# Performance work log

Measured on AMD Instinct MI355X. Metric: run time of the kernel, lower is better.

The kernel has to match this reference:

```python
import jax, jax.numpy as jnp
import numpy as np

FP32_MIN_NORMAL = 2.0 ** -126
BLOCK = 128
STD_DEV = 2.0
# inlier format int4: ebits=0, mbits=4+2, emax=0, max_norm=(2^5-1)/2^4
EBITS_IN, MBITS_IN, EMAX_IN, MAXNORM_IN = 0, 6, 0, (2 ** 5 - 1) / 2 ** 4
# outlier format fp8_e4m3: ebits=4, mbits=3+2, emax=2^3, max_norm=2^8*1.75
EBITS_OUT, MBITS_OUT, EMAX_OUT, MAXNORM_OUT = 4, 5, 8, 448.0
SCALE_EMAX = 2 ** (8 - 1) - 1  # inlier/outlier scale_bits = 8
SCALE_LO = -20.0  # original: lower clamp is -20 because -scale_emax < -20


def setup_inputs():
    key = jax.random.key(0)
    x = jax.random.normal(key, (4096, 8192), dtype=jnp.float32)
    return {"x": x}


def _quantize_elemwise(A, mbits, ebits, max_norm):
    # faithful to microxcaling _quantize_elemwise_core with allow_denorm=True,
    # saturate_normals=True, round='nearest' (finite inputs assumed)
    if ebits != 0:
        pexp = jnp.floor(jnp.log2(jnp.abs(A) + (A == 0).astype(A.dtype)))
        pexp = jnp.maximum(pexp, float(-(2 ** (ebits - 1)) + 2))
        scale = jnp.exp2(float(mbits - 2) - pexp)
    else:
        scale = float(2 ** (mbits - 2))
    out = A * scale
    out = jnp.sign(out) * jnp.floor(jnp.abs(out) + 0.5)  # round-to-nearest
    out = out / scale
    return jnp.clip(out, -max_norm, max_norm)


def _shared_exp(A):
    # max-abs over the block axis, then floor(log2(.)), zero-safe
    m = jnp.max(jnp.abs(A), axis=-1, keepdims=True)
    return jnp.floor(jnp.log2(m + FP32_MIN_NORMAL * (m == 0).astype(m.dtype)))


def _clamp_scale(se):
    se = jnp.where(se > SCALE_EMAX, jnp.nan, se)  # never triggers for fp32-range data
    return jnp.where(se < -SCALE_EMAX, SCALE_LO, se)


def _quantize_mx_outlier(x):
    R, C = x.shape  # C divisible by BLOCK -> no padding branch
    A = x.reshape(R, C // BLOCK, BLOCK)
    # outlier detection: mean/std of |A| per block (population std), bounds vs A
    absA = jnp.abs(A)
    mean = jnp.mean(absA, axis=-1, keepdims=True)
    std = jnp.sqrt(jnp.mean((absA - mean) ** 2, axis=-1, keepdims=True))
    outlier = ((A < mean - STD_DEV * std) | (A > mean + STD_DEV * std)).astype(A.dtype)
    inlier_val = A * (1.0 - outlier)
    outlier_val = A * outlier
    # inlier shared exponent + quantize
    se_in = _clamp_scale(_shared_exp(inlier_val) - EMAX_IN)
    s_in = jnp.exp2(se_in)
    inlier_val = _quantize_elemwise(inlier_val / s_in, MBITS_IN, EBITS_IN, MAXNORM_IN) * s_in
    # outlier path (note: scaled UP by inlier scale, as in original)
    outlier_val = outlier_val * s_in
    se_out = _clamp_scale(_shared_exp(outlier_val) - EMAX_OUT)
    s_out = jnp.exp2(se_out)
    outlier_val = _quantize_elemwise(outlier_val / s_out, MBITS_OUT, EBITS_OUT, MAXNORM_OUT) * s_out / s_in
    return (inlier_val + outlier_val).reshape(R, C)


def reference(x):
    return _quantize_mx_outlier(x)
```

## Files before the change

kernel.cpp:

```cpp
#include <hip/hip_runtime.h>

typedef float f32x4 __attribute__((ext_vector_type(4)));

__device__ __forceinline__ int flog2_exact(float x) {
    unsigned b = __float_as_uint(x);
    int e = (int)((b >> 23) & 0xFFu);
    if (e == 0) {
        unsigned m = b & 0x7FFFFFu;
        return 31 - __clz(m) - 149;
    }
    return e - 127;
}

__device__ __forceinline__ float round_ref(float v) {
    return copysignf(floorf(fabsf(v) + 0.5f), v);
}

__global__ __launch_bounds__(256) void mxq_kernel(const f32x4* __restrict__ x,
                                                  f32x4* __restrict__ y,
                                                  int ntask) {
    const int lane = threadIdx.x & 63;
    const int l    = lane & 15;
    const int q    = lane >> 4;
    const int wid  = blockIdx.x * (blockDim.x >> 6) + (threadIdx.x >> 6);
    const int nw   = gridDim.x * (blockDim.x >> 6);

    for (int t = wid; t < ntask; t += nw) {
        const size_t base = (size_t)t * 128 + q * 32 + l;
        const f32x4 v0 = x[base];
        const f32x4 v1 = x[base + 16];
        float a[8] = {v0.x, v0.y, v0.z, v0.w, v1.x, v1.y, v1.z, v1.w};

        double s = 0.0, s2 = 0.0;
        #pragma unroll
        for (int i = 0; i < 8; ++i) {
            double d = (double)fabsf(a[i]);
            s += d;
            s2 = fma(d, d, s2);
        }
        #pragma unroll
        for (int off = 1; off < 16; off <<= 1) {
            s  += __shfl_xor(s, off);
            s2 += __shfl_xor(s2, off);
        }
        const double mean = s * (1.0 / 128.0);
        double var = fma(mean, -mean, s2 * (1.0 / 128.0));
        var = var < 0.0 ? 0.0 : var;
        const double v4 = 4.0 * var;

        bool o[8];
        float mi = 0.0f, mov = 0.0f;
        #pragma unroll
        for (int i = 0; i < 8; ++i) {
            double dd = (double)a[i] - mean;
            o[i] = fma(dd, dd, -v4) > 0.0;
            float ab = fabsf(a[i]);
            mi  = fmaxf(mi,  o[i] ? 0.0f : ab);
            mov = fmaxf(mov, o[i] ? ab : 0.0f);
        }
        #pragma unroll
        for (int off = 1; off < 16; off <<= 1) {
            mi  = fmaxf(mi,  __shfl_xor(mi, off));
            mov = fmaxf(mov, __shfl_xor(mov, off));
        }

        int se_in = (mi == 0.0f) ? -126 : flog2_exact(mi);
        if (se_in < -127) se_in = -20;
        int se_out = ((mov == 0.0f) ? -126 : (flog2_exact(mov) + se_in)) - 8;
        if (se_out < -127) se_out = -20;
        const int d   = se_in - se_out;
        const int g_in = se_in - 4;
        const float L_in  = ldexpf(31.0f, g_in);
        const float L_out = ldexpf(448.0f, -d);
        const int d3 = d + 3;

        f32x4 r0, r1;
        #pragma unroll
        for (int i = 0; i < 8; ++i) {
            int e_a = (int)((__float_as_uint(a[i]) >> 23) & 0xFFu) - 127;
            int pe  = e_a + d;
            pe = pe < -6 ? -6 : pe;
            int g = o[i] ? (pe - d3) : g_in;
            float r    = round_ref(ldexpf(a[i], -g));
            float outv = ldexpf(r, g);
            float L    = o[i] ? L_out : L_in;
            outv = fminf(fmaxf(outv, -L), L);
            if (i < 4) r0[i] = outv; else r1[i - 4] = outv;
        }

        __builtin_nontemporal_store(r0, &y[base]);
        __builtin_nontemporal_store(r1, &y[base + 16]);
    }
}

extern "C" void kernel_launch(void* const* d_in, const int* in_sizes, int n_in,
                              void* d_out, int out_size, void* d_ws, size_t ws_size,
                              hipStream_t stream) {
    const f32x4* x = (const f32x4*)d_in[0];
    f32x4* y = (f32x4*)d_out;
    int n = in_sizes[0];
    int ntask = n / 512;
    int threads = 256;
    int waves_per_wg = threads / 64;
    int grid = 2048;
    int max_grid = (ntask + waves_per_wg - 1) / waves_per_wg;
    if (grid > max_grid) grid = max_grid;
    mxq_kernel<<<grid, threads, 0, stream>>>(x, y, ntask);
}
```

Measured before the change: 46.07 us.

## Process two tasks per wave iteration with register double-buffered prefetch

Each wave now handles a super-task of two 128-element rows per iteration (8 f32x4 loads in flight) and prefetches the next super-task's data into registers before computing the current one. The aim is to hide global memory latency in this bandwidth-bound kernel and raise memory-level parallelism per wave. The cost is higher register pressure, which may lower occupancy, and half as many tasks to spread across waves.

```diff
diff --git a/kernel.cpp b/kernel.cpp
--- a/kernel.cpp
+++ b/kernel.cpp
@@ -16,80 +16,101 @@
     return copysignf(floorf(fabsf(v) + 0.5f), v);
 }
 
+__device__ __forceinline__ void process_task(const f32x4 v0, const f32x4 v1,
+                                             f32x4& r0, f32x4& r1) {
+    float a[8] = {v0.x, v0.y, v0.z, v0.w, v1.x, v1.y, v1.z, v1.w};
+
+    double s = 0.0, s2 = 0.0;
+    #pragma unroll
+    for (int i = 0; i < 8; ++i) {
+        double d = (double)fabsf(a[i]);
+        s += d;
+        s2 = fma(d, d, s2);
+    }
+    #pragma unroll
+    for (int off = 1; off < 16; off <<= 1) {
+        s  += __shfl_xor(s, off);
+        s2 += __shfl_xor(s2, off);
+    }
+    const double mean = s * (1.0 / 128.0);
+    double var = fma(mean, -mean, s2 * (1.0 / 128.0));
+    var = var < 0.0 ? 0.0 : var;
+    const double v4 = 4.0 * var;
+
+    bool o[8];
+    float mi = 0.0f, mov = 0.0f;
+    #pragma unroll
+    for (int i = 0; i < 8; ++i) {
+        double dd = (double)a[i] - mean;
+        o[i] = fma(dd, dd, -v4) > 0.0;
+        float ab = fabsf(a[i]);
+        mi  = fmaxf(mi,  o[i] ? 0.0f : ab);
+        mov = fmaxf(mov, o[i] ? ab : 0.0f);
+    }
+    #pragma unroll
+    for (int off = 1; off < 16; off <<= 1) {
+        mi  = fmaxf(mi,  __shfl_xor(mi, off));
+        mov = fmaxf(mov, __shfl_xor(mov, off));
+    }
+
+    int se_in = (mi == 0.0f) ? -126 : flog2_exact(mi);
+    if (se_in < -127) se_in = -20;
+    int se_out = ((mov == 0.0f) ? -126 : (flog2_exact(mov) + se_in)) - 8;
+    if (se_out < -127) se_out = -20;
+    const int d   = se_in - se_out;
+    const int g_in = se_in - 4;
+    const float L_in  = ldexpf(31.0f, g_in);
+    const float L_out = ldexpf(448.0f, -d);
+    const int d3 = d + 3;
+
+    #pragma unroll
+    for (int i = 0; i < 8; ++i) {
+        int e_a = (int)((__float_as_uint(a[i]) >> 23) & 0xFFu) - 127;
+        int pe  = e_a + d;
+        pe = pe < -6 ? -6 : pe;
+        int g = o[i] ? (pe - d3) : g_in;
+        float r    = round_ref(ldexpf(a[i], -g));
+        float outv = ldexpf(r, g);
+        float L    = o[i] ? L_out : L_in;
+        outv = fminf(fmaxf(outv, -L), L);
+        if (i < 4) r0[i] = outv; else r1[i - 4] = outv;
+    }
+}
+
 __global__ __launch_bounds__(256) void mxq_kernel(const f32x4* __restrict__ x,
                                                   f32x4* __restrict__ y,
-                                                  int ntask) {
+                                                  int nsuper) {
     const int lane = threadIdx.x & 63;
-    const int l    = lane & 15;
-    const int q    = lane >> 4;
+    const int off0 = (lane >> 4) * 32 + (lane & 15);
     const int wid  = blockIdx.x * (blockDim.x >> 6) + (threadIdx.x >> 6);
     const int nw   = gridDim.x * (blockDim.x >> 6);
 
-    for (int t = wid; t < ntask; t += nw) {
-        const size_t base = (size_t)t * 128 + q * 32 + l;
-        const f32x4 v0 = x[base];
-        const f32x4 v1 = x[base + 16];
-        float a[8] = {v0.x, v0.y, v0.z, v0.w, v1.x, v1.y, v1.z, v1.w};
-
-        double s = 0.0, s2 = 0.0;
-        #pragma unroll
-        for (int i = 0; i < 8; ++i) {
-            double d = (double)fabsf(a[i]);
-            s += d;
-            s2 = fma(d, d, s2);
-        }
-        #pragma unroll
-        for (int off = 1; off < 16; off <<= 1) {
-            s  += __shfl_xor(s, off);
-            s2 += __shfl_xor(s2, off);
-        }
-        const double mean = s * (1.0 / 128.0);
-        double var = fma(mean, -mean, s2 * (1.0 / 128.0));
-        var = var < 0.0 ? 0.0 : var;
-        const double v4 = 4.0 * var;
-
-        bool o[8];
-        float mi = 0.0f, mov = 0.0f;
-        #pragma unroll
-        for (int i = 0; i < 8; ++i) {
-            double dd = (double)a[i] - mean;
-            o[i] = fma(dd, dd, -v4) > 0.0;
-            float ab = fabsf(a[i]);
-            mi  = fmaxf(mi,  o[i] ? 0.0f : ab);
-            mov = fmaxf(mov, o[i] ? ab : 0.0f);
-        }
-        #pragma unroll
-        for (int off = 1; off < 16; off <<= 1) {
-            mi  = fmaxf(mi,  __shfl_xor(mi, off));
-            mov = fmaxf(mov, __shfl_xor(mov, off));
+    int t = wid;
+    f32x4 d0, d1, d2, d3;
+    if (t < nsuper) {
+        const size_t b = (size_t)t * 256 + off0;
+        d0 = x[b]; d1 = x[b + 16]; d2 = x[b + 128]; d3 = x[b + 144];
+    }
+    while (t < nsuper) {
+        const int tn = t + nw;
+        f32x4 e0 = d0, e1 = d1, e2 = d2, e3 = d3;
+        if (tn < nsuper) {
+            const size_t bn = (size_t)tn * 256 + off0;
+            e0 = x[bn]; e1 = x[bn + 16]; e2 = x[bn + 128]; e3 = x[bn + 144];
         }
 
-        int se_in = (mi == 0.0f) ? -126 : flog2_exact(mi);
-        if (se_in < -127) se_in = -20;
-        int se_out = ((mov == 0.0f) ? -126 : (flog2_exact(mov) + se_in)) - 8;
-        if (se_out < -127) se_out = -20;
-        const int d   = se_in - se_out;
-        const int g_in = se_in - 4;
-        const float L_in  = ldexpf(31.0f, g_in);
-        const float L_out = ldexpf(448.0f, -d);
-        const int d3 = d + 3;
+        f32x4 r0, r1, r2, r3;
+        process_task(d0, d1, r0, r1);
+        process_task(d2, d3, r2, r3);
 
-        f32x4 r0, r1;
-        #pragma unroll
-        for (int i = 0; i < 8; ++i) {
-            int e_a = (int)((__float_as_uint(a[i]) >> 23) & 0xFFu) - 127;
-            int pe  = e_a + d;
-            pe = pe < -6 ? -6 : pe;
-            int g = o[i] ? (pe - d3) : g_in;
-            float r    = round_ref(ldexpf(a[i], -g));
-            float outv = ldexpf(r, g);
-            float L    = o[i] ? L_out : L_in;
-            outv = fminf(fmaxf(outv, -L), L);
-            if (i < 4) r0[i] = outv; else r1[i - 4] = outv;
-        }
+        const size_t b = (size_t)t * 256 + off0;
+        __builtin_nontemporal_store(r0, &y[b]);
+        __builtin_nontemporal_store(r1, &y[b + 16]);
+        __builtin_nontemporal_store(r2, &y[b + 128]);
+        __builtin_nontemporal_store(r3, &y[b + 144]);
 
-        __builtin_nontemporal_store(r0, &y[base]);
-        __builtin_nontemporal_store(r1, &y[base + 16]);
+        d0 = e0; d1 = e1; d2 = e2; d3 = e3;
+        t = tn;
     }
 }
 
@@ -99,11 +120,11 @@
     const f32x4* x = (const f32x4*)d_in[0];
     f32x4* y = (f32x4*)d_out;
     int n = in_sizes[0];
-    int ntask = n / 512;
+    int nsuper = n / 1024;
     int threads = 256;
     int waves_per_wg = threads / 64;
     int grid = 2048;
-    int max_grid = (ntask + waves_per_wg - 1) / waves_per_wg;
+    int max_grid = (nsuper + waves_per_wg - 1) / waves_per_wg;
     if (grid > max_grid) grid = max_grid;
-    mxq_kernel<<<grid, threads, 0, stream>>>(x, y, ntask);
+    mxq_kernel<<<grid, threads, 0, stream>>>(x, y, nsuper);
 }
```

New measurement: 48.62 us. +5.5%, slower.
